# Performance work log

Hardware: AMD Instinct MI355X
Metric: run time of the kernel (lower is better)

## Reference

```python
import jax, jax.numpy as jnp
import numpy as np

EPS = 1e-8  # numerical guard in padded (masked) softmax denominator


def setup_inputs() -> dict:
    key = jax.random.key(0)
    k1, k2 = jax.random.split(key)
    B, N, D = 8, 2048, 3
    coordinates = jax.random.normal(k1, (B, N, D), dtype=jnp.float32)
    masks = (jax.random.uniform(k2, (B, N, N)) < 0.9).astype(jnp.float32)
    sigma = jnp.ones((1,), dtype=jnp.float32)  # NonNeg learned scalar
    return {"coordinates": coordinates, "masks": masks, "sigma": sigma}


def reference(coordinates, masks, sigma):
    # pairwise squared euclidean distances: ||xi||^2 - 2 xi.xj + ||xj||^2
    norms = jnp.sum(coordinates ** 2, axis=-1, keepdims=True)            # [B,N,1]
    inner = jnp.einsum('bnd,bmd->bnm', coordinates, coordinates)         # [B,N,N]
    distances = norms - 2.0 * inner + jnp.swapaxes(norms, -1, -2)        # [B,N,N]
    # Gaussian kernel
    A = jnp.exp(-distances / (sigma ** 2))                               # [B,N,N]
    # padded_softmax: mask then row-normalize (A is positive, so this is a
    # masked softmax over -d/sigma^2 along the last axis)
    A = A * masks
    return A / (jnp.sum(A, axis=-1, keepdims=True) + EPS)
```

## Files before the change

kernel.cpp:

```cpp
#include <hip/hip_runtime.h>
#include <math.h>


#define NN      2048
#define THREADS 512
#define EPS     1e-8f

typedef float vf4 __attribute__((ext_vector_type(4)));

__global__ __launch_bounds__(THREADS, 8) void gauss_adj_kernel(
    const float* __restrict__ coords,
    const float* __restrict__ masks,
    const float* __restrict__ sigma,
    float* __restrict__ out)
{
    const int tid = threadIdx.x;
    const int rib = tid >> 8;
    const int tir = tid & 255;
    const int row = blockIdx.x * 2 + rib;
    const int b   = row >> 11;
    const int i   = row & (NN - 1);

    __shared__ __align__(16) float qx[NN];
    __shared__ __align__(16) float qy[NN];
    __shared__ __align__(16) float qz[NN];
    __shared__ __align__(16) float qw[NN];
    __shared__ float red[8];

    const float s = sigma[0];
    const float C = 1.44269504088896341f / (s * s);
    const float* cb = coords + (size_t)b * NN * 3;

    for (int idx = tid; idx < NN; idx += THREADS) {
        const float x = cb[idx * 3 + 0];
        const float y = cb[idx * 3 + 1];
        const float z = cb[idx * 3 + 2];
        qx[idx] = 2.0f * C * x;
        qy[idx] = 2.0f * C * y;
        qz[idx] = 2.0f * C * z;
        qw[idx] = -C * (x * x + y * y + z * z);
    }
    __syncthreads();

    const float xi = cb[i * 3 + 0];
    const float yi = cb[i * 3 + 1];
    const float zi = cb[i * 3 + 2];

    const vf4* mrow = (const vf4*)(masks + (size_t)row * NN);
    vf4*       orow = (vf4*)(out + (size_t)row * NN);
    const vf4* qx4 = (const vf4*)qx;
    const vf4* qy4 = (const vf4*)qy;
    const vf4* qz4 = (const vf4*)qz;
    const vf4* qw4 = (const vf4*)qw;

    vf4 m0 = mrow[tir];
    vf4 m1 = mrow[256 + tir];

    float lsum = 0.0f;

#define DOCHUNK(M, Q) { \
        const int q_ = (Q); \
        const vf4 X = qx4[q_], Y = qy4[q_], Z = qz4[q_], W = qw4[q_]; \
        M.x *= exp2f(fmaf(xi, X.x, fmaf(yi, Y.x, fmaf(zi, Z.x, W.x)))); \
        M.y *= exp2f(fmaf(xi, X.y, fmaf(yi, Y.y, fmaf(zi, Z.y, W.y)))); \
        M.z *= exp2f(fmaf(xi, X.z, fmaf(yi, Y.z, fmaf(zi, Z.z, W.z)))); \
        M.w *= exp2f(fmaf(xi, X.w, fmaf(yi, Y.w, fmaf(zi, Z.w, W.w)))); \
        lsum += (M.x + M.y) + (M.z + M.w); \
    }

    DOCHUNK(m0, tir)
    DOCHUNK(m1, 256 + tir)
#undef DOCHUNK

    #pragma unroll
    for (int off = 32; off > 0; off >>= 1)
        lsum += __shfl_xor(lsum, off, 64);
    if ((tid & 63) == 0) red[tid >> 6] = lsum;
    __syncthreads();
    const int rb = rib * 4;
    const float tot = (red[rb] + red[rb + 1]) + (red[rb + 2] + red[rb + 3]);
    const float inv = 1.0f / (tot + EPS);

    m0.x *= inv; m0.y *= inv; m0.z *= inv; m0.w *= inv;
    m1.x *= inv; m1.y *= inv; m1.z *= inv; m1.w *= inv;
    __builtin_nontemporal_store(m0, &orow[tir]);
    __builtin_nontemporal_store(m1, &orow[256 + tir]);
}

extern "C" void kernel_launch(void* const* d_in, const int* in_sizes, int n_in,
                              void* d_out, int out_size, void* d_ws, size_t ws_size,
                              hipStream_t stream) {
    const float* coords = (const float*)d_in[0];
    const float* masks  = (const float*)d_in[1];
    const float* sigma  = (const float*)d_in[2];
    float* out = (float*)d_out;

    const int B    = in_sizes[0] / (NN * 3);
    const int rows = B * NN;
    gauss_adj_kernel<<<rows / 2, THREADS, 0, stream>>>(coords, masks, sigma, out);
}
```

Before: 238.9 us.

## Assign one row per wavefront and process sixteen rows per block

Each wavefront now owns a whole row: it loads all 8 vf4 chunks of the mask row, computes the Gaussian terms, and reduces the sum with shuffles only. This removes the shared-memory block reduction and its __syncthreads. Each block handles 16 rows in two passes, so the per-batch shared-memory table of transformed coordinates is built once for 16 rows instead of 2. The cost is more registers per thread and 8x fewer blocks, which may lower occupancy and reduce latency hiding for a memory-bound kernel.

```diff
diff --git a/kernel.cpp b/kernel.cpp
--- a/kernel.cpp
+++ b/kernel.cpp
@@ -4,6 +4,7 @@
 
 #define NN      2048
 #define THREADS 512
+#define ROWS_PER_BLOCK 16
 #define EPS     1e-8f
 
 typedef float vf4 __attribute__((ext_vector_type(4)));
@@ -14,77 +15,80 @@
     const float* __restrict__ sigma,
     float* __restrict__ out)
 {
-    const int tid = threadIdx.x;
-    const int rib = tid >> 8;
-    const int tir = tid & 255;
-    const int row = blockIdx.x * 2 + rib;
-    const int b   = row >> 11;
-    const int i   = row & (NN - 1);
+    const int tid  = threadIdx.x;
+    const int wid  = tid >> 6;
+    const int lane = tid & 63;
+    const int base = blockIdx.x * ROWS_PER_BLOCK;
+    const int b    = base >> 11;
 
     __shared__ __align__(16) float qx[NN];
     __shared__ __align__(16) float qy[NN];
     __shared__ __align__(16) float qz[NN];
     __shared__ __align__(16) float qw[NN];
-    __shared__ float red[8];
 
     const float s = sigma[0];
     const float C = 1.44269504088896341f / (s * s);
+    const float twoC = 2.0f * C;
     const float* cb = coords + (size_t)b * NN * 3;
 
     for (int idx = tid; idx < NN; idx += THREADS) {
         const float x = cb[idx * 3 + 0];
         const float y = cb[idx * 3 + 1];
         const float z = cb[idx * 3 + 2];
-        qx[idx] = 2.0f * C * x;
-        qy[idx] = 2.0f * C * y;
-        qz[idx] = 2.0f * C * z;
+        qx[idx] = twoC * x;
+        qy[idx] = twoC * y;
+        qz[idx] = twoC * z;
         qw[idx] = -C * (x * x + y * y + z * z);
     }
     __syncthreads();
 
-    const float xi = cb[i * 3 + 0];
-    const float yi = cb[i * 3 + 1];
-    const float zi = cb[i * 3 + 2];
-
-    const vf4* mrow = (const vf4*)(masks + (size_t)row * NN);
-    vf4*       orow = (vf4*)(out + (size_t)row * NN);
     const vf4* qx4 = (const vf4*)qx;
     const vf4* qy4 = (const vf4*)qy;
     const vf4* qz4 = (const vf4*)qz;
     const vf4* qw4 = (const vf4*)qw;
 
-    vf4 m0 = mrow[tir];
-    vf4 m1 = mrow[256 + tir];
+    #pragma unroll
+    for (int g = 0; g < 2; ++g) {
+        const int row = base + (g << 3) + wid;
+        const int i   = row & (NN - 1);
 
-    float lsum = 0.0f;
+        const float xi = cb[i * 3 + 0];
+        const float yi = cb[i * 3 + 1];
+        const float zi = cb[i * 3 + 2];
 
-#define DOCHUNK(M, Q) { \
-        const int q_ = (Q); \
-        const vf4 X = qx4[q_], Y = qy4[q_], Z = qz4[q_], W = qw4[q_]; \
-        M.x *= exp2f(fmaf(xi, X.x, fmaf(yi, Y.x, fmaf(zi, Z.x, W.x)))); \
-        M.y *= exp2f(fmaf(xi, X.y, fmaf(yi, Y.y, fmaf(zi, Z.y, W.y)))); \
-        M.z *= exp2f(fmaf(xi, X.z, fmaf(yi, Y.z, fmaf(zi, Z.z, W.z)))); \
-        M.w *= exp2f(fmaf(xi, X.w, fmaf(yi, Y.w, fmaf(zi, Z.w, W.w)))); \
-        lsum += (M.x + M.y) + (M.z + M.w); \
+        const vf4* mrow = (const vf4*)(masks + (size_t)row * NN);
+        vf4*       orow = (vf4*)(out + (size_t)row * NN);
+
+        vf4 a[8];
+        #pragma unroll
+        for (int w = 0; w < 8; ++w) a[w] = mrow[w * 64 + lane];
+
+        float lsum = 0.0f;
+        #pragma unroll
+        for (int w = 0; w < 8; ++w) {
+            const int q_ = w * 64 + lane;
+            const vf4 X = qx4[q_], Y = qy4[q_], Z = qz4[q_], W = qw4[q_];
+            vf4 v = a[w];
+            v.x *= exp2f(fmaf(xi, X.x, fmaf(yi, Y.x, fmaf(zi, Z.x, W.x))));
+            v.y *= exp2f(fmaf(xi, X.y, fmaf(yi, Y.y, fmaf(zi, Z.y, W.y))));
+            v.z *= exp2f(fmaf(xi, X.z, fmaf(yi, Y.z, fmaf(zi, Z.z, W.z))));
+            v.w *= exp2f(fmaf(xi, X.w, fmaf(yi, Y.w, fmaf(zi, Z.w, W.w))));
+            a[w] = v;
+            lsum += (v.x + v.y) + (v.z + v.w);
+        }
+
+        #pragma unroll
+        for (int off = 32; off > 0; off >>= 1)
+            lsum += __shfl_xor(lsum, off, 64);
+        const float inv = 1.0f / (lsum + EPS);
+
+        #pragma unroll
+        for (int w = 0; w < 8; ++w) {
+            vf4 o = a[w];
+            o.x *= inv; o.y *= inv; o.z *= inv; o.w *= inv;
+            __builtin_nontemporal_store(o, &orow[w * 64 + lane]);
+        }
     }
-
-    DOCHUNK(m0, tir)
-    DOCHUNK(m1, 256 + tir)
-#undef DOCHUNK
-
-    #pragma unroll
-    for (int off = 32; off > 0; off >>= 1)
-        lsum += __shfl_xor(lsum, off, 64);
-    if ((tid & 63) == 0) red[tid >> 6] = lsum;
-    __syncthreads();
-    const int rb = rib * 4;
-    const float tot = (red[rb] + red[rb + 1]) + (red[rb + 2] + red[rb + 3]);
-    const float inv = 1.0f / (tot + EPS);
-
-    m0.x *= inv; m0.y *= inv; m0.z *= inv; m0.w *= inv;
-    m1.x *= inv; m1.y *= inv; m1.z *= inv; m1.w *= inv;
-    __builtin_nontemporal_store(m0, &orow[tir]);
-    __builtin_nontemporal_store(m1, &orow[256 + tir]);
 }
 
 extern "C" void kernel_launch(void* const* d_in, const int* in_sizes, int n_in,
@@ -97,5 +101,5 @@
 
     const int B    = in_sizes[0] / (NN * 3);
     const int rows = B * NN;
-    gauss_adj_kernel<<<rows / 2, THREADS, 0, stream>>>(coords, masks, sigma, out);
+    gauss_adj_kernel<<<rows / ROWS_PER_BLOCK, THREADS, 0, stream>>>(coords, masks, sigma, out);
 }
```

After: 274.3 us. +14.8%, slower.
